# Kernel optimization log

Hardware: AMD Instinct MI355X
Metric: run time of the kernel (lower is better)

Reference implementation:

```python
import jax, jax.numpy as jnp
import numpy as np

BOTTLENECK_DIM = 128
TOP_K = 8
SCALE = 1.0 / np.sqrt(BOTTLENECK_DIM)
EPS = 1e-10


def setup_inputs() -> dict:
    key = jax.random.key(0)
    k1, k2, k3, k4 = jax.random.split(key, 4)
    query = jax.random.normal(k1, (4, 4096, 128), dtype=jnp.float32)
    keys = jax.random.normal(k2, (4096, 128), dtype=jnp.float32)
    values = jax.random.normal(k3, (4096, 1024), dtype=jnp.float32)
    reliability = jax.random.uniform(k4, (4096,), dtype=jnp.float32)
    return {"query": query, "keys": keys, "values": values, "reliability": reliability}


def reference(query, keys, values, reliability):
    # Routing: [b, s, num_slots] scores with log-reliability bias, take top-k slots.
    router_scores = jnp.einsum("bsd,nd->bsn", query, keys) + jnp.log(reliability + EPS)
    _, top_indices = jax.lax.top_k(router_scores, TOP_K)  # [b, s, k]

    # Gather per-token slot keys/values: [b, s, k, d] and [b, s, k, h]
    selected_keys = keys[top_indices]
    selected_values = values[top_indices]

    # Small-k attention over gathered slots.
    attn_scores = jnp.einsum("bsd,bskd->bsk", query, selected_keys) * SCALE
    attn_weights = jax.nn.softmax(attn_scores, axis=-1)  # [b, s, k]
    output = jnp.einsum("bsk,bskh->bsh", attn_weights, selected_values)
    return output, attn_weights
```

## Files before the change

kernel.cpp:

```cpp
#include <hip/hip_runtime.h>
#include <hip/hip_fp16.h>
#include <math.h>

#define NSLOTS 4096
#define DIM    128
#define HDIM   1024
#define NTOK   16384
#define SCALE  0.08838834764831845f
#define REPS   1e-10f

typedef __attribute__((ext_vector_type(8))) short bf16x8;
typedef __attribute__((ext_vector_type(4))) float f32x4;

typedef __attribute__((address_space(1))) const void* as1cv;
typedef __attribute__((address_space(3))) void* as3v;

__device__ __forceinline__ float pack_score(float biased, unsigned inv_idx) {
    return __uint_as_float((__float_as_uint(biased) & 0xFFFFF000u) | inv_idx);
}
#define PACK_NEG_INF __uint_as_float(0xFF7FF000u)

__device__ __forceinline__ void ins_packed(float (&r)[8], float x) {
    #pragma unroll
    for (int i = 0; i < 7; ++i) r[i] = __builtin_amdgcn_fmed3f(r[i], x, r[i + 1]);
    r[7] = fmaxf(r[7], x);
}

__device__ __forceinline__ void merge_out16(float (&r)[8], int kseg, float* outS) {
    float hv = r[7];
    #pragma unroll
    for (int rnd = 0; rnd < 16; ++rnd) {
        float bv = hv;
        bv = fmaxf(bv, __shfl_xor(bv, 16, 64));
        bv = fmaxf(bv, __shfl_xor(bv, 32, 64));
        if ((rnd >> 2) == kseg) outS[rnd] = bv;
        if (hv == bv) {
            #pragma unroll
            for (int m2 = 7; m2 > 0; --m2) r[m2] = r[m2 - 1];
            r[0] = PACK_NEG_INF;
            hv = r[7];
        }
    }
}

__device__ __forceinline__ ushort f2bf(float f) {
    unsigned u = __float_as_uint(f);
    return (ushort)((u + 0x7fffu + ((u >> 16) & 1u)) >> 16);
}
#define QB_N  524288
#define KBP_N 65536
#define LR_N  4096
#define VH_N  524288
__global__ void prep_kernel(const float* __restrict__ q, const float* __restrict__ k,
                            const float* __restrict__ rel, const float* __restrict__ v,
                            ushort* __restrict__ qb, ushort* __restrict__ kbp,
                            float* __restrict__ lr, ushort* __restrict__ vh) {
    int gid = blockIdx.x * 256 + threadIdx.x;
    if (gid < QB_N) {
        float4 vv = ((const float4*)q)[gid];
        ushort4 o; o.x = f2bf(vv.x); o.y = f2bf(vv.y); o.z = f2bf(vv.z); o.w = f2bf(vv.w);
        ((ushort4*)qb)[gid] = o;
    } else if (gid < QB_N + KBP_N) {
        int C = gid - QB_N;
        int l = C & 63, kc = (C >> 6) & 3, t16 = C >> 8;
        int slot = t16 * 16 + (l & 15);
        int doff = kc * 32 + (l >> 4) * 8;
        const float4* src = (const float4*)(k + (size_t)slot * DIM + doff);
        float4 v0 = src[0], v1 = src[1];
        union { ushort u[8]; uint4 v; } o;
        o.u[0] = f2bf(v0.x); o.u[1] = f2bf(v0.y); o.u[2] = f2bf(v0.z); o.u[3] = f2bf(v0.w);
        o.u[4] = f2bf(v1.x); o.u[5] = f2bf(v1.y); o.u[6] = f2bf(v1.z); o.u[7] = f2bf(v1.w);
        ((uint4*)kbp)[C] = o.v;
    } else if (gid < QB_N + KBP_N + LR_N) {
        int g = gid - QB_N - KBP_N;
        lr[g] = logf(rel[g] + REPS);
    } else if (gid < QB_N + KBP_N + LR_N + VH_N) {
        int g = gid - QB_N - KBP_N - LR_N;
        const float4* src = (const float4*)v + (size_t)g * 2;
        float4 a = src[0], b = src[1];
        union { _Float16 h[8]; uint4 u; } o;
        o.h[0] = (_Float16)a.x; o.h[1] = (_Float16)a.y;
        o.h[2] = (_Float16)a.z; o.h[3] = (_Float16)a.w;
        o.h[4] = (_Float16)b.x; o.h[5] = (_Float16)b.y;
        o.h[6] = (_Float16)b.z; o.h[7] = (_Float16)b.w;
        ((uint4*)vh)[g] = o.u;
    }
}

__launch_bounds__(256, 4)
__global__ void route_kernel(const ushort* __restrict__ qb,
                             const ushort* __restrict__ kbp,
                             const float*  __restrict__ lr,
                             int* __restrict__ cand) {
    __shared__ ushort ktile[4][2][4 * 512];
    __shared__ float  qS[16][4][16];
    const int tid  = threadIdx.x;
    const int lane = tid & 63;
    const int q    = tid >> 6;
    const int m    = lane & 15;
    const int kseg = lane >> 4;
    const int tokbase = blockIdx.x * 16;

    bf16x8 bF[4];
    const ushort* qrow = qb + (size_t)(tokbase + m) * DIM + kseg * 8;
    #pragma unroll
    for (int kc = 0; kc < 4; ++kc)
        bF[kc] = *(const bf16x8*)(qrow + kc * 32);

    float R[8];
    #pragma unroll
    for (int i = 0; i < 8; ++i) R[i] = PACK_NEG_INF;

    auto issue = [&](int t, int buf) {
        const ushort* gt = kbp + ((size_t)((q * 64 + t) * 256 + lane)) * 8;
        ushort* lb = &ktile[q][buf][0];
        #pragma unroll
        for (int i = 0; i < 4; ++i) {
            __builtin_amdgcn_global_load_lds((as1cv)(gt + i * 512),
                                             (as3v)(lb + i * 512 + lane * 8), 16, 0, 0);
        }
    };

    issue(0, 0);
    __syncthreads();

    for (int t = 0; t < 64; ++t) {
        const int cur = t & 1;
        if (t < 63) issue(t + 1, 1 - cur);

        const ushort* kt = &ktile[q][cur][0];
        f32x4 acc = {0.f, 0.f, 0.f, 0.f};
        #pragma unroll
        for (int kc = 0; kc < 4; ++kc) {
            bf16x8 aF = *(const bf16x8*)(kt + kc * 512 + lane * 8);
            acc = __builtin_amdgcn_mfma_f32_16x16x32_bf16(aF, bF[kc], acc, 0, 0, 0);
        }
        const int base = q * 1024 + t * 16;
        float4 lrv = ((const float4*)lr)[(base >> 2) + kseg];
        unsigned invb = 4095u - (unsigned)(base + kseg * 4);
        ins_packed(R, pack_score(acc[0] + lrv.x, invb));
        ins_packed(R, pack_score(acc[1] + lrv.y, invb - 1));
        ins_packed(R, pack_score(acc[2] + lrv.z, invb - 2));
        ins_packed(R, pack_score(acc[3] + lrv.w, invb - 3));
        __syncthreads();
    }

    merge_out16(R, kseg, &qS[m][q][0]);
    __syncthreads();

    if (tid < 16) {
        const int token = tokbase + tid;
        int p[4] = {0, 0, 0, 0};
        #pragma unroll
        for (int c = 0; c < 16; ++c) {
            float bv = -INFINITY; int bq = 0;
            #pragma unroll
            for (int j = 0; j < 4; ++j) {
                float v = (p[j] < 16) ? qS[tid][j][p[j]] : -INFINITY;
                if (v > bv) { bv = v; bq = j; }
            }
            cand[(size_t)token * 16 + c] = 4095 - (int)(__float_as_uint(bv) & 0xFFFu);
            ++p[bq];
        }
    }
}

__device__ __forceinline__ float2 h2f2(unsigned u) {
    return __half22float2(*reinterpret_cast<const __half2*>(&u));
}
__launch_bounds__(256)
__global__ void rescue_gather_kernel(const float* __restrict__ query,
                                     const float* __restrict__ keys,
                                     const float* __restrict__ lr,
                                     const int*   __restrict__ cand,
                                     const ushort* __restrict__ vh,
                                     float* __restrict__ out,
                                     float* __restrict__ wout) {
    const int tid  = threadIdx.x;
    const int w    = tid >> 6;
    const int lane = tid & 63;
    const int token = blockIdx.x * 4 + w;
    const int c  = lane >> 2;
    const int qp = lane & 3;

    int ci = cand[(size_t)token * 16 + c];
    const float4* q4 = (const float4*)(query + (size_t)token * DIM) + qp * 8;
    const float4* k4 = (const float4*)(keys  + (size_t)ci    * DIM) + qp * 8;
    float sum = 0.f;
    #pragma unroll
    for (int i = 0; i < 8; ++i) {
        float4 a = q4[i], b = k4[i];
        sum = fmaf(a.x, b.x, sum); sum = fmaf(a.y, b.y, sum);
        sum = fmaf(a.z, b.z, sum); sum = fmaf(a.w, b.w, sum);
    }
    sum += __shfl_xor(sum, 1, 4);
    sum += __shfl_xor(sum, 2, 4);
    float raw = sum;
    float s   = sum + lr[ci];

    float rsel[8]; int isel[8];
    #pragma unroll
    for (int rnd = 0; rnd < 8; ++rnd) {
        float bv = s; int bi = ci; float br = raw;
        #pragma unroll
        for (int off = 4; off < 64; off <<= 1) {
            float ov  = __shfl_xor(bv, off, 64);
            int   oi  = __shfl_xor(bi, off, 64);
            float orr = __shfl_xor(br, off, 64);
            if (ov > bv || (ov == bv && oi < bi)) { bv = ov; bi = oi; br = orr; }
        }
        rsel[rnd] = br; isel[rnd] = bi;
        if (s == bv && ci == bi) s = -INFINITY;
    }

    float mx = -INFINITY;
    #pragma unroll
    for (int k = 0; k < 8; ++k) { rsel[k] *= SCALE; mx = fmaxf(mx, rsel[k]); }
    float e[8]; float ssum = 0.f;
    #pragma unroll
    for (int k = 0; k < 8; ++k) { e[k] = expf(rsel[k] - mx); ssum += e[k]; }
    float inv = 1.0f / ssum;
    float wk[8];
    #pragma unroll
    for (int k = 0; k < 8; ++k) wk[k] = e[k] * inv;

    if (lane == 0) {
        #pragma unroll
        for (int k = 0; k < 8; ++k) wout[(size_t)token * 8 + k] = wk[k];
    }

    float oA[8], oB[8];
    #pragma unroll
    for (int i = 0; i < 8; ++i) { oA[i] = 0.f; oB[i] = 0.f; }
    #pragma unroll
    for (int k = 0; k < 8; ++k) {
        const uint4* vr = (const uint4*)vh + (size_t)isel[k] * 128;
        float wkk = wk[k];
        uint4 va = vr[lane];
        uint4 vb = vr[lane + 64];
        float2 f;
        f = h2f2(va.x); oA[0] = fmaf(wkk, f.x, oA[0]); oA[1] = fmaf(wkk, f.y, oA[1]);
        f = h2f2(va.y); oA[2] = fmaf(wkk, f.x, oA[2]); oA[3] = fmaf(wkk, f.y, oA[3]);
        f = h2f2(va.z); oA[4] = fmaf(wkk, f.x, oA[4]); oA[5] = fmaf(wkk, f.y, oA[5]);
        f = h2f2(va.w); oA[6] = fmaf(wkk, f.x, oA[6]); oA[7] = fmaf(wkk, f.y, oA[7]);
        f = h2f2(vb.x); oB[0] = fmaf(wkk, f.x, oB[0]); oB[1] = fmaf(wkk, f.y, oB[1]);
        f = h2f2(vb.y); oB[2] = fmaf(wkk, f.x, oB[2]); oB[3] = fmaf(wkk, f.y, oB[3]);
        f = h2f2(vb.z); oB[4] = fmaf(wkk, f.x, oB[4]); oB[5] = fmaf(wkk, f.y, oB[5]);
        f = h2f2(vb.w); oB[6] = fmaf(wkk, f.x, oB[6]); oB[7] = fmaf(wkk, f.y, oB[7]);
    }
    float4* orow = (float4*)(out + (size_t)token * HDIM);
    orow[lane * 2]           = make_float4(oA[0], oA[1], oA[2], oA[3]);
    orow[lane * 2 + 1]       = make_float4(oA[4], oA[5], oA[6], oA[7]);
    orow[128 + lane * 2]     = make_float4(oB[0], oB[1], oB[2], oB[3]);
    orow[128 + lane * 2 + 1] = make_float4(oB[4], oB[5], oB[6], oB[7]);
}

extern "C" void kernel_launch(void* const* d_in, const int* in_sizes, int n_in,
                              void* d_out, int out_size, void* d_ws, size_t ws_size,
                              hipStream_t stream) {
    const float* query  = (const float*)d_in[0];
    const float* keys   = (const float*)d_in[1];
    const float* values = (const float*)d_in[2];
    const float* rel    = (const float*)d_in[3];

    float* out  = (float*)d_out;
    float* wout = out + (size_t)NTOK * HDIM;

    char* ws = (char*)d_ws;
    float*  lr   = (float*)ws;   ws += 4096 * 4;
    ushort* qb   = (ushort*)ws;  ws += (size_t)NTOK * DIM * 2;
    ushort* kbp  = (ushort*)ws;  ws += (size_t)NSLOTS * DIM * 2;
    int*    cand = (int*)ws;     ws += (size_t)NTOK * 16 * 4;
    ushort* vh   = (ushort*)ws;

    int prep_grid = (QB_N + KBP_N + LR_N + VH_N) / 256;
    hipLaunchKernelGGL(prep_kernel, dim3(prep_grid), dim3(256), 0, stream,
                       query, keys, rel, values, qb, kbp, lr, vh);
    hipLaunchKernelGGL(route_kernel, dim3(NTOK / 16), dim3(256), 0, stream,
                       qb, kbp, lr, cand);
    hipLaunchKernelGGL(rescue_gather_kernel, dim3(NTOK / 4), dim3(256), 0, stream,
                       query, keys, lr, cand, vh, out, wout);
}
```

Baseline: 203.3 us.

## Route 32 tokens per block from register-prefetched keys; bitonic sort rescue candidates

The routing kernel now handles 32 tokens per 512-thread block with 8 waves, each scanning 512 slots. Key tiles are double-buffered in registers straight from global memory, replacing the LDS global_load_lds staging and the per-iteration __syncthreads. Each loaded key fragment feeds two MFMAs, one per 16-token group, which halves key traffic per token at the cost of more registers for two top-8 lists. In the rescue kernel, the 8-round shuffle argmax selection is replaced by a bitonic sort across the 16 candidates.

```diff
diff --git a/kernel.cpp b/kernel.cpp
--- a/kernel.cpp
+++ b/kernel.cpp
@@ -11,9 +11,6 @@
 
 typedef __attribute__((ext_vector_type(8))) short bf16x8;
 typedef __attribute__((ext_vector_type(4))) float f32x4;
-
-typedef __attribute__((address_space(1))) const void* as1cv;
-typedef __attribute__((address_space(3))) void* as3v;
 
 __device__ __forceinline__ float pack_score(float biased, unsigned inv_idx) {
     return __uint_as_float((__float_as_uint(biased) & 0xFFFFF000u) | inv_idx);
@@ -87,75 +84,81 @@
     }
 }
 
-__launch_bounds__(256, 4)
+__launch_bounds__(512, 4)
 __global__ void route_kernel(const ushort* __restrict__ qb,
                              const ushort* __restrict__ kbp,
                              const float*  __restrict__ lr,
                              int* __restrict__ cand) {
-    __shared__ ushort ktile[4][2][4 * 512];
-    __shared__ float  qS[16][4][16];
+    __shared__ float qS[32][8][17];
     const int tid  = threadIdx.x;
     const int lane = tid & 63;
-    const int q    = tid >> 6;
+    const int w    = tid >> 6;
     const int m    = lane & 15;
     const int kseg = lane >> 4;
-    const int tokbase = blockIdx.x * 16;
-
-    bf16x8 bF[4];
-    const ushort* qrow = qb + (size_t)(tokbase + m) * DIM + kseg * 8;
+    const int tokbase = blockIdx.x * 32;
+
+    bf16x8 bF0[4], bF1[4];
+    const ushort* q0 = qb + (size_t)(tokbase + m) * DIM + kseg * 8;
+    const ushort* q1 = qb + (size_t)(tokbase + 16 + m) * DIM + kseg * 8;
+    #pragma unroll
+    for (int kc = 0; kc < 4; ++kc) {
+        bF0[kc] = *(const bf16x8*)(q0 + kc * 32);
+        bF1[kc] = *(const bf16x8*)(q1 + kc * 32);
+    }
+
+    float R0[8], R1[8];
+    #pragma unroll
+    for (int i = 0; i < 8; ++i) { R0[i] = PACK_NEG_INF; R1[i] = PACK_NEG_INF; }
+
+    const uint4* kb4 = (const uint4*)kbp;
+    const int tbase = w * 32;
+
+    uint4 A[4], N[4];
     #pragma unroll
     for (int kc = 0; kc < 4; ++kc)
-        bF[kc] = *(const bf16x8*)(qrow + kc * 32);
-
-    float R[8];
-    #pragma unroll
-    for (int i = 0; i < 8; ++i) R[i] = PACK_NEG_INF;
-
-    auto issue = [&](int t, int buf) {
-        const ushort* gt = kbp + ((size_t)((q * 64 + t) * 256 + lane)) * 8;
-        ushort* lb = &ktile[q][buf][0];
-        #pragma unroll
-        for (int i = 0; i < 4; ++i) {
-            __builtin_amdgcn_global_load_lds((as1cv)(gt + i * 512),
-                                             (as3v)(lb + i * 512 + lane * 8), 16, 0, 0);
-        }
-    };
-
-    issue(0, 0);
-    __syncthreads();
-
-    for (int t = 0; t < 64; ++t) {
-        const int cur = t & 1;
-        if (t < 63) issue(t + 1, 1 - cur);
-
-        const ushort* kt = &ktile[q][cur][0];
-        f32x4 acc = {0.f, 0.f, 0.f, 0.f};
+        A[kc] = kb4[(size_t)tbase * 256 + kc * 64 + lane];
+
+    for (int t = 0; t < 32; ++t) {
+        if (t < 31) {
+            #pragma unroll
+            for (int kc = 0; kc < 4; ++kc)
+                N[kc] = kb4[(size_t)(tbase + t + 1) * 256 + kc * 64 + lane];
+        }
+        f32x4 acc0 = {0.f, 0.f, 0.f, 0.f};
+        f32x4 acc1 = {0.f, 0.f, 0.f, 0.f};
         #pragma unroll
         for (int kc = 0; kc < 4; ++kc) {
-            bf16x8 aF = *(const bf16x8*)(kt + kc * 512 + lane * 8);
-            acc = __builtin_amdgcn_mfma_f32_16x16x32_bf16(aF, bF[kc], acc, 0, 0, 0);
-        }
-        const int base = q * 1024 + t * 16;
+            bf16x8 aF = *(const bf16x8*)&A[kc];
+            acc0 = __builtin_amdgcn_mfma_f32_16x16x32_bf16(aF, bF0[kc], acc0, 0, 0, 0);
+            acc1 = __builtin_amdgcn_mfma_f32_16x16x32_bf16(aF, bF1[kc], acc1, 0, 0, 0);
+        }
+        const int base = w * 512 + t * 16;
         float4 lrv = ((const float4*)lr)[(base >> 2) + kseg];
         unsigned invb = 4095u - (unsigned)(base + kseg * 4);
-        ins_packed(R, pack_score(acc[0] + lrv.x, invb));
-        ins_packed(R, pack_score(acc[1] + lrv.y, invb - 1));
-        ins_packed(R, pack_score(acc[2] + lrv.z, invb - 2));
-        ins_packed(R, pack_score(acc[3] + lrv.w, invb - 3));
-        __syncthreads();
-    }
-
-    merge_out16(R, kseg, &qS[m][q][0]);
+        ins_packed(R0, pack_score(acc0[0] + lrv.x, invb));
+        ins_packed(R0, pack_score(acc0[1] + lrv.y, invb - 1));
+        ins_packed(R0, pack_score(acc0[2] + lrv.z, invb - 2));
+        ins_packed(R0, pack_score(acc0[3] + lrv.w, invb - 3));
+        ins_packed(R1, pack_score(acc1[0] + lrv.x, invb));
+        ins_packed(R1, pack_score(acc1[1] + lrv.y, invb - 1));
+        ins_packed(R1, pack_score(acc1[2] + lrv.z, invb - 2));
+        ins_packed(R1, pack_score(acc1[3] + lrv.w, invb - 3));
+        #pragma unroll
+        for (int kc = 0; kc < 4; ++kc) A[kc] = N[kc];
+    }
+
+    merge_out16(R0, kseg, &qS[m][w][0]);
+    merge_out16(R1, kseg, &qS[m + 16][w][0]);
     __syncthreads();
 
-    if (tid < 16) {
+    if (tid < 32) {
         const int token = tokbase + tid;
-        int p[4] = {0, 0, 0, 0};
+        int p[8] = {0, 0, 0, 0, 0, 0, 0, 0};
         #pragma unroll
         for (int c = 0; c < 16; ++c) {
             float bv = -INFINITY; int bq = 0;
             #pragma unroll
-            for (int j = 0; j < 4; ++j) {
+            for (int j = 0; j < 8; ++j) {
                 float v = (p[j] < 16) ? qS[tid][j][p[j]] : -INFINITY;
                 if (v > bv) { bv = v; bq = j; }
             }
@@ -198,19 +201,26 @@
     float raw = sum;
     float s   = sum + lr[ci];
 
+    #pragma unroll
+    for (int k = 2; k <= 16; k <<= 1) {
+        #pragma unroll
+        for (int j = k >> 1; j >= 1; j >>= 1) {
+            int off = j << 2;
+            float s2 = __shfl_xor(s,   off, 64);
+            float r2 = __shfl_xor(raw, off, 64);
+            int   i2 = __shfl_xor(ci,  off, 64);
+            bool mineFirst = (s > s2) || (s == s2 && ci < i2);
+            bool lower = (c & j) == 0;
+            bool asc   = (c & k) == 0;
+            bool keep  = (lower == asc) ? mineFirst : !mineFirst;
+            if (!keep) { s = s2; raw = r2; ci = i2; }
+        }
+    }
     float rsel[8]; int isel[8];
     #pragma unroll
-    for (int rnd = 0; rnd < 8; ++rnd) {
-        float bv = s; int bi = ci; float br = raw;
-        #pragma unroll
-        for (int off = 4; off < 64; off <<= 1) {
-            float ov  = __shfl_xor(bv, off, 64);
-            int   oi  = __shfl_xor(bi, off, 64);
-            float orr = __shfl_xor(br, off, 64);
-            if (ov > bv || (ov == bv && oi < bi)) { bv = ov; bi = oi; br = orr; }
-        }
-        rsel[rnd] = br; isel[rnd] = bi;
-        if (s == bv && ci == bi) s = -INFINITY;
+    for (int r = 0; r < 8; ++r) {
+        rsel[r] = __shfl(raw, r * 4, 64);
+        isel[r] = __shfl(ci,  r * 4, 64);
     }
 
     float mx = -INFINITY;
@@ -276,7 +286,7 @@
     int prep_grid = (QB_N + KBP_N + LR_N + VH_N) / 256;
     hipLaunchKernelGGL(prep_kernel, dim3(prep_grid), dim3(256), 0, stream,
                        query, keys, rel, values, qb, kbp, lr, vh);
-    hipLaunchKernelGGL(route_kernel, dim3(NTOK / 16), dim3(256), 0, stream,
+    hipLaunchKernelGGL(route_kernel, dim3(NTOK / 32), dim3(512), 0, stream,
                        qb, kbp, lr, cand);
     hipLaunchKernelGGL(rescue_gather_kernel, dim3(NTOK / 4), dim3(256), 0, stream,
                        query, keys, lr, cand, vh, out, wout);
```

Result: faster. 188.1 us (median of 2 runs) (-7.5%).
